# Kernel optimization log

Hardware: AMD Instinct MI355X
Metric: run time of the kernel (lower is better)

## Reference

```python
import jax, jax.numpy as jnp
import numpy as np

INPUT_WIDTH = 256
DEPTH = 7
OUTPUT_WIDTH = 256
N_NODES = 2 ** (DEPTH + 1) - 1  # 255


def setup_inputs() -> dict:
    key = jax.random.key(0)
    k_x, k_w1, k_w2 = jax.random.split(key, 3)
    init1 = 1.0 / np.sqrt(INPUT_WIDTH)
    x = jax.random.normal(k_x, (2, 1024, INPUT_WIDTH), dtype=jnp.float32)
    w1s = jax.random.uniform(k_w1, (N_NODES, INPUT_WIDTH), jnp.float32, -init1, init1)
    b1s = jnp.zeros((N_NODES,), jnp.float32)
    w2s = jax.random.uniform(k_w2, (N_NODES, INPUT_WIDTH, OUTPUT_WIDTH), jnp.float32, -init1, init1)
    b2s = jnp.zeros((N_NODES, OUTPUT_WIDTH), jnp.float32)
    return {"x": x, "w1s": w1s, "b1s": b1s, "w2s": w2s, "b2s": b2s}


def reference(x, w1s, b1s, w2s, b2s):
    B, S, D = x.shape
    flat_x = x.reshape(B * S, D)  # [T, D]
    T = flat_x.shape[0]

    # --- routing pass: walk the binary tree, recording node ids and logits ---
    current = jnp.zeros((T,), dtype=jnp.int32)
    all_nodes = []
    all_logits = []
    for _ in range(DEPTH + 1):
        all_nodes.append(current)
        score = jnp.einsum('td,td->t', flat_x, w1s[current]) + b1s[current]  # [T]
        all_logits.append(score)
        # ((sign+1)/2).long(): sign(0)->0 maps to choice 0 via truncation
        choice = ((jnp.sign(score) + 1.0) / 2.0).astype(jnp.int32)
        current = current * 2 + choice + 1

    logits = jnp.stack(all_logits, axis=1)  # [T, DEPTH+1]
    path_weights = jax.nn.gelu(jnp.abs(logits), approximate=False)  # exact erf GELU

    # --- output pass: weighted sum of per-node transforms along the path ---
    out = jnp.zeros((T, OUTPUT_WIDTH), dtype=x.dtype)
    for i in range(DEPTH + 1):
        nodes_i = all_nodes[i]
        t_i = jnp.einsum('td,tdo->to', flat_x, w2s[nodes_i]) + b2s[nodes_i]  # [T, O]
        out = out + t_i * path_weights[:, i][:, None]

    return out.reshape(B, S, OUTPUT_WIDTH)
```

## Files before the change

kernel.cpp:

```cpp
#include <hip/hip_runtime.h>
#include <hip/hip_bf16.h>

#define T_TOKENS 2048
#define DIM 256
#define NLEV 8

using bf16x8 = __attribute__((ext_vector_type(8))) short;
using f32x4  = __attribute__((ext_vector_type(4))) float;

__device__ __forceinline__ unsigned short f2bf(float f) {
    union { float f; unsigned u; } v; v.f = f;
    unsigned r = v.u + 0x7FFFu + ((v.u >> 16) & 1u);
    return (unsigned short)(r >> 16);
}

__global__ __launch_bounds__(256) void route_kernel(
    const float* __restrict__ x, const float* __restrict__ w1s,
    const float* __restrict__ b1s,
    float* __restrict__ pw,
    int*   __restrict__ pc)
{
    int wave = threadIdx.x >> 6;
    int lane = threadIdx.x & 63;
    int t = blockIdx.x * 4 + wave;

    const float4 xv = *reinterpret_cast<const float4*>(x + (size_t)t * DIM + lane * 4);
    int p = 1;
    float keep = 0.0f;
    #pragma unroll
    for (int lvl = 0; lvl < NLEV; ++lvl) {
        int node = p - 1;
        const float4 wv = *reinterpret_cast<const float4*>(w1s + (size_t)node * DIM + lane * 4);
        float s = xv.x * wv.x + xv.y * wv.y + xv.z * wv.z + xv.w * wv.w;
        #pragma unroll
        for (int off = 32; off; off >>= 1) s += __shfl_xor(s, off);
        float score = s + b1s[node];
        float a = fabsf(score);
        float g = a * 0.5f * (1.0f + erff(a * 0.70710678118654752f));
        if (lane == lvl) keep = g;
        int choice = (score > 0.0f) ? 1 : 0;
        p = 2 * p + choice;
    }
    if (lane < NLEV) pw[(size_t)t * NLEV + lane] = keep;
    if (lane == 0) pc[t] = p;
}

__global__ __launch_bounds__(256) void sort_kernel(
    const int* __restrict__ pc,
    int* __restrict__ order, unsigned* __restrict__ units, int* __restrict__ ucount)
{
    __shared__ int hist[256];
    __shared__ int offs[256];
    __shared__ int cums[257];
    __shared__ int wpart[4];
    int tid = threadIdx.x;
    hist[tid] = 0;
    __syncthreads();

    int myPc[8];
    #pragma unroll
    for (int i = 0; i < 8; ++i) {
        int t = tid * 8 + i;
        myPc[i] = pc[t];
        atomicAdd(&hist[myPc[i] - 256], 1);
    }
    __syncthreads();

    if (tid < 64) {
        int lane = tid;
        int v0 = hist[lane * 4 + 0], v1 = hist[lane * 4 + 1];
        int v2 = hist[lane * 4 + 2], v3 = hist[lane * 4 + 3];
        int sum = v0 + v1 + v2 + v3;
        int scan = sum;
        #pragma unroll
        for (int off = 1; off < 64; off <<= 1) {
            int n = __shfl_up(scan, off);
            if (lane >= off) scan += n;
        }
        int excl = scan - sum;
        offs[lane * 4 + 0] = excl;
        offs[lane * 4 + 1] = excl + v0;
        offs[lane * 4 + 2] = excl + v0 + v1;
        offs[lane * 4 + 3] = excl + v0 + v1 + v2;
    }
    __syncthreads();

    cums[tid] = offs[tid];
    if (tid == 0) cums[256] = T_TOKENS;
    __syncthreads();

    #pragma unroll
    for (int i = 0; i < 8; ++i) {
        int t = tid * 8 + i;
        int bin = myPc[i] - 256;
        int pos = atomicAdd(&offs[bin], 1);
        order[pos] = t;
    }

    int nch = 0, s = 0, e = 0, l = 0;
    if (tid < 255) {
        int q = tid + 1;
        l = 31 - __clz(q);
        int shift = 8 - l;
        int lo = (q << shift) - 256;
        int hi = ((q + 1) << shift) - 256;
        s = cums[lo];
        e = cums[hi];
        nch = (e - s + 63) >> 6;
    }
    int lane = tid & 63, w = tid >> 6;
    int scan = nch;
    #pragma unroll
    for (int off = 1; off < 64; off <<= 1) {
        int n = __shfl_up(scan, off);
        if (lane >= off) scan += n;
    }
    if (lane == 63) wpart[w] = scan;
    __syncthreads();
    int pre = 0;
    for (int k = 0; k < w; ++k) pre += wpart[k];
    int base = pre + scan - nch;
    for (int j = 0; j < nch; ++j) {
        int st = s + j * 64;
        int c = e - st; if (c > 64) c = 64;
        units[base + j] = (unsigned)tid | ((unsigned)l << 8) |
                          ((unsigned)st << 11) | ((unsigned)c << 22);
    }
    if (tid == 255) *ucount = pre + scan;
}

__global__ __launch_bounds__(256, 3) void out_kernel(
    const float* __restrict__ x, const float* __restrict__ w2s,
    const float* __restrict__ b2s, const float* __restrict__ pw,
    const int* __restrict__ order, const unsigned* __restrict__ units,
    const int* __restrict__ ucount, float* __restrict__ lvlbuf)
{
    __shared__ unsigned short As[16384];
    __shared__ unsigned short Bs[2][4096];

    int u = blockIdx.x >> 1;
    int ch = blockIdx.x & 1;
    if (u >= *ucount) return;
    unsigned d = units[u];
    int node  = (int)(d & 255u);
    int lvl   = (int)((d >> 8) & 7u);
    int start = (int)((d >> 11) & 2047u);
    int cnt   = (int)((d >> 22) & 127u);

    int tid = threadIdx.x;
    int wv = tid >> 6, lane = tid & 63;
    int l15 = lane & 15, kg = lane >> 4;

    const float* w2n = w2s + ((size_t)node << 16) + ch * 128;

    float2 La0[8], La1[8];
    auto loadB = [&](int p, float2 (&La)[8]) {
        const float* bp = w2n + (size_t)(p * 32 + wv * 8) * DIM + lane * 2;
        #pragma unroll
        for (int j = 0; j < 8; ++j)
            La[j] = *reinterpret_cast<const float2*>(bp + (size_t)j * DIM);
    };
    auto writeB = [&](unsigned short* bs, const float2 (&La)[8]) {
        bf16x8 v0, v1;
        #pragma unroll
        for (int j = 0; j < 8; ++j) {
            v0[j] = (short)f2bf(La[j].x);
            v1[j] = (short)f2bf(La[j].y);
        }
        int g0 = wv * 128 + lane * 2;
        int g1 = g0 + 1;
        *reinterpret_cast<bf16x8*>(&bs[(g0 ^ ((g0 >> 3) & 7)) * 8]) = v0;
        *reinterpret_cast<bf16x8*>(&bs[(g1 ^ ((g1 >> 3) & 7)) * 8]) = v1;
    };

    loadB(0, La0);
    loadB(1, La1);

    {
        int r = tid >> 2, seg = tid & 3;
        if (r < cnt) {
            int t = order[start + r];
            const float* xp = x + (size_t)t * DIM + seg * 64;
            #pragma unroll
            for (int g = 0; g < 8; ++g) {
                float4 a0 = *reinterpret_cast<const float4*>(xp + g * 8);
                float4 a1 = *reinterpret_cast<const float4*>(xp + g * 8 + 4);
                bf16x8 v;
                v[0] = (short)f2bf(a0.x); v[1] = (short)f2bf(a0.y);
                v[2] = (short)f2bf(a0.z); v[3] = (short)f2bf(a0.w);
                v[4] = (short)f2bf(a1.x); v[5] = (short)f2bf(a1.y);
                v[6] = (short)f2bf(a1.z); v[7] = (short)f2bf(a1.w);
                int gk = seg * 8 + g;
                int gg = r * 32 + (gk ^ (r & 7));
                *reinterpret_cast<bf16x8*>(&As[gg * 8]) = v;
            }
        }
    }
    writeB(Bs[0], La0);
    __syncthreads();

    f32x4 acc[4][2];
    #pragma unroll
    for (int m = 0; m < 4; ++m)
        #pragma unroll
        for (int nb = 0; nb < 2; ++nb) acc[m][nb] = (f32x4){0.f, 0.f, 0.f, 0.f};

    #pragma unroll
    for (int p = 0; p < 8; ++p) {
        if (p < 6) {
            if (p & 1) loadB(p + 2, La1); else loadB(p + 2, La0);
        }
        unsigned short* bs = Bs[p & 1];
        bf16x8 a[4], b[2];
        #pragma unroll
        for (int nb = 0; nb < 2; ++nb) {
            int g = kg * 128 + wv * 32 + nb * 16 + l15;
            b[nb] = *reinterpret_cast<bf16x8*>(&bs[(g ^ ((g >> 3) & 7)) * 8]);
        }
        #pragma unroll
        for (int m = 0; m < 4; ++m) if (m * 16 < cnt) {
            int row = m * 16 + l15;
            int g = row * 32 + ((p * 4 + kg) ^ (row & 7));
            a[m] = *reinterpret_cast<bf16x8*>(&As[g * 8]);
        }
        #pragma unroll
        for (int m = 0; m < 4; ++m) if (m * 16 < cnt)
            #pragma unroll
            for (int nb = 0; nb < 2; ++nb)
                acc[m][nb] = __builtin_amdgcn_mfma_f32_16x16x32_bf16(a[m], b[nb], acc[m][nb], 0, 0, 0);
        if (p < 7) {
            if (p & 1) writeB(Bs[(p + 1) & 1], La0); else writeB(Bs[(p + 1) & 1], La1);
        }
        __syncthreads();
    }

    float bias[2];
    #pragma unroll
    for (int nb = 0; nb < 2; ++nb)
        bias[nb] = b2s[((size_t)node << 8) + ch * 128 + wv * 32 + nb * 16 + l15];

    float* dst = lvlbuf + ((size_t)lvl << 19);

    #pragma unroll
    for (int m = 0; m < 4; ++m) if (m * 16 < cnt) {
        #pragma unroll
        for (int j = 0; j < 4; ++j) {
            int r = m * 16 + kg * 4 + j;
            if (r < cnt) {
                int t = order[start + r];
                float w = pw[(size_t)t * NLEV + lvl];
                #pragma unroll
                for (int nb = 0; nb < 2; ++nb) {
                    float val = w * (acc[m][nb][j] + bias[nb]);
                    dst[(size_t)t * DIM + ch * 128 + wv * 32 + nb * 16 + l15] = val;
                }
            }
        }
    }
}

__global__ __launch_bounds__(256) void reduce_kernel(
    const float* __restrict__ lvlbuf, float* __restrict__ out)
{
    int idx = blockIdx.x * 256 + threadIdx.x;
    const float4* lb = reinterpret_cast<const float4*>(lvlbuf);
    float4 s = lb[idx];
    #pragma unroll
    for (int l = 1; l < NLEV; ++l) {
        float4 v = lb[(size_t)l * 131072 + idx];
        s.x += v.x; s.y += v.y; s.z += v.z; s.w += v.w;
    }
    reinterpret_cast<float4*>(out)[idx] = s;
}

extern "C" void kernel_launch(void* const* d_in, const int* in_sizes, int n_in,
                              void* d_out, int out_size, void* d_ws, size_t ws_size,
                              hipStream_t stream) {
    const float* x   = (const float*)d_in[0];
    const float* w1s = (const float*)d_in[1];
    const float* b1s = (const float*)d_in[2];
    const float* w2s = (const float*)d_in[3];
    const float* b2s = (const float*)d_in[4];
    float* out = (float*)d_out;

    float* pw       = (float*)d_ws;
    int* pc         = (int*)(pw + T_TOKENS * NLEV);
    int* order      = pc + T_TOKENS;
    unsigned* units = (unsigned*)(order + T_TOKENS);
    int* ucount     = (int*)(units + 512);
    float* lvlbuf   = (float*)((char*)d_ws + (1 << 20));

    route_kernel<<<T_TOKENS / 4, 256, 0, stream>>>(x, w1s, b1s, pw, pc);
    sort_kernel<<<1, 256, 0, stream>>>(pc, order, units, ucount);
    out_kernel<<<1024, 256, 0, stream>>>(x, w2s, b2s, pw, order, units, ucount, lvlbuf);
    reduce_kernel<<<512, 256, 0, stream>>>(lvlbuf, out);
}
```

Measured before the change: 46.20 us.

## Give each wave a private B tile so the K loop drops block barriers

Reorganizes the W2 staging so each wave loads, converts and stores only the 32 output columns it consumes into its own shared-memory slice. Because no wave reads another wave's B data, the per-iteration __syncthreads in the K loop is removed, leaving one barrier after the shared A tile is built. Global loads change from float2-per-lane rows to scalar column-strided loads, which may reduce coalescing width. Correctness relies on intra-wave ordering of LDS writes and reads within the double buffer.

Result: faster. 45.04 us (-2.5%).

```diff
diff --git a/kernel.cpp b/kernel.cpp
--- a/kernel.cpp
+++ b/kernel.cpp
@@ -136,7 +136,7 @@
     const int* __restrict__ ucount, float* __restrict__ lvlbuf)
 {
     __shared__ unsigned short As[16384];
-    __shared__ unsigned short Bs[2][4096];
+    __shared__ unsigned short BsW[4][2][1024];
 
     int u = blockIdx.x >> 1;
     int ch = blockIdx.x & 1;
@@ -151,30 +151,31 @@
     int wv = tid >> 6, lane = tid & 63;
     int l15 = lane & 15, kg = lane >> 4;
 
-    const float* w2n = w2s + ((size_t)node << 16) + ch * 128;
-
-    float2 La0[8], La1[8];
-    auto loadB = [&](int p, float2 (&La)[8]) {
-        const float* bp = w2n + (size_t)(p * 32 + wv * 8) * DIM + lane * 2;
-        #pragma unroll
-        for (int j = 0; j < 8; ++j)
-            La[j] = *reinterpret_cast<const float2*>(bp + (size_t)j * DIM);
+    const float* w2c = w2s + ((size_t)node << 16) + ch * 128 + wv * 32 + (lane & 31);
+    int rg = (lane >> 5) * 8;
+
+    float Ra[16], Rb[16];
+    auto loadB = [&](int p, float (&R)[16]) {
+        const float* bp = w2c + (size_t)(p * 32 + rg) * DIM;
+        #pragma unroll
+        for (int i = 0; i < 8; ++i) R[i] = bp[(size_t)i * DIM];
+        #pragma unroll
+        for (int i = 0; i < 8; ++i) R[8 + i] = bp[(size_t)(16 + i) * DIM];
     };
-    auto writeB = [&](unsigned short* bs, const float2 (&La)[8]) {
+    auto writeB = [&](int q, const float (&R)[16]) {
         bf16x8 v0, v1;
         #pragma unroll
-        for (int j = 0; j < 8; ++j) {
-            v0[j] = (short)f2bf(La[j].x);
-            v1[j] = (short)f2bf(La[j].y);
-        }
-        int g0 = wv * 128 + lane * 2;
-        int g1 = g0 + 1;
-        *reinterpret_cast<bf16x8*>(&bs[(g0 ^ ((g0 >> 3) & 7)) * 8]) = v0;
-        *reinterpret_cast<bf16x8*>(&bs[(g1 ^ ((g1 >> 3) & 7)) * 8]) = v1;
+        for (int i = 0; i < 8; ++i) { v0[i] = (short)f2bf(R[i]); v1[i] = (short)f2bf(R[8 + i]); }
+        int gi0 = lane;
+        int gi1 = lane + 64;
+        int s0 = gi0 ^ ((gi0 >> 3) & 7);
+        int s1 = gi1 ^ ((gi1 >> 3) & 7);
+        *reinterpret_cast<bf16x8*>(&BsW[wv][q][s0 * 8]) = v0;
+        *reinterpret_cast<bf16x8*>(&BsW[wv][q][s1 * 8]) = v1;
     };
 
-    loadB(0, La0);
-    loadB(1, La1);
+    loadB(0, Ra);
+    loadB(1, Rb);
 
     {
         int r = tid >> 2, seg = tid & 3;
@@ -196,7 +197,7 @@
             }
         }
     }
-    writeB(Bs[0], La0);
+    writeB(0, Ra);
     __syncthreads();
 
     f32x4 acc[4][2];
@@ -208,14 +209,14 @@
     #pragma unroll
     for (int p = 0; p < 8; ++p) {
         if (p < 6) {
-            if (p & 1) loadB(p + 2, La1); else loadB(p + 2, La0);
-        }
-        unsigned short* bs = Bs[p & 1];
+            if (p & 1) loadB(p + 2, Rb); else loadB(p + 2, Ra);
+        }
         bf16x8 a[4], b[2];
         #pragma unroll
         for (int nb = 0; nb < 2; ++nb) {
-            int g = kg * 128 + wv * 32 + nb * 16 + l15;
-            b[nb] = *reinterpret_cast<bf16x8*>(&bs[(g ^ ((g >> 3) & 7)) * 8]);
+            int gi = kg * 32 + nb * 16 + l15;
+            int si = gi ^ ((gi >> 3) & 7);
+            b[nb] = *reinterpret_cast<bf16x8*>(&BsW[wv][p & 1][si * 8]);
         }
         #pragma unroll
         for (int m = 0; m < 4; ++m) if (m * 16 < cnt) {
@@ -229,9 +230,8 @@
             for (int nb = 0; nb < 2; ++nb)
                 acc[m][nb] = __builtin_amdgcn_mfma_f32_16x16x32_bf16(a[m], b[nb], acc[m][nb], 0, 0, 0);
         if (p < 7) {
-            if (p & 1) writeB(Bs[(p + 1) & 1], La0); else writeB(Bs[(p + 1) & 1], La1);
-        }
-        __syncthreads();
+            if (p & 1) writeB((p + 1) & 1, Ra); else writeB((p + 1) & 1, Rb);
+        }
     }
 
     float bias[2];
```
